# Kernel tuning notes

Measured on AMD Instinct MI355X. Metric: run time of the kernel, lower is better.

## Reference

```python
import jax, jax.numpy as jnp
import numpy as np
import math

D_INPUT = 1024
D_Q = 1024
D_K = 1024
D_V = 1024
D_MODEL = 1024
B, S = 4, 2048


def setup_inputs() -> dict:
    key = jax.random.key(0)
    ks = jax.random.split(key, 9)
    sc = 0.02
    return {
        "x": jax.random.normal(ks[0], (B, S, D_INPUT), dtype=jnp.float32),
        "wq": jax.random.normal(ks[1], (D_INPUT, D_Q), dtype=jnp.float32) * sc,
        "bq": jnp.zeros((D_Q,), dtype=jnp.float32),
        "wk": jax.random.normal(ks[2], (D_INPUT, D_K), dtype=jnp.float32) * sc,
        "bk": jnp.zeros((D_K,), dtype=jnp.float32),
        "wv": jax.random.normal(ks[3], (D_INPUT, D_V), dtype=jnp.float32) * sc,
        "bv": jnp.zeros((D_V,), dtype=jnp.float32),
        "wp": jax.random.normal(ks[4], (D_V, D_MODEL), dtype=jnp.float32) * sc,
        "bp": jnp.zeros((D_MODEL,), dtype=jnp.float32),
    }


def reference(x, wq, bq, wk, bk, wv, bv, wp, bp):
    scale = math.sqrt(D_K)  # NOTE: original MULTIPLIES by sqrt(d_k)
    q = x @ wq + bq  # [B,S,Dq]
    k = x @ wk + bk  # [B,S,Dk]
    v = x @ wv + bv  # [B,S,Dv]
    scores = jnp.einsum('bsd,btd->bst', q, k) * scale
    p_attn = jax.nn.softmax(scores, axis=-1)
    # dropout: inference mode (training=False) -> identity
    context = jnp.einsum('bst,btd->bsd', p_attn, v)
    output = context @ wp + bp
    return (output, p_attn)
```

## Files before the change

kernel.cpp:

```cpp
#include <hip/hip_runtime.h>

typedef unsigned short u16;
typedef short bf16x8 __attribute__((ext_vector_type(8)));
typedef float floatx4 __attribute__((ext_vector_type(4)));

static __device__ __forceinline__ u16 f2bf(float f) {
  unsigned int u = __float_as_uint(f);
  unsigned int lsb = (u >> 16) & 1u;
  u += 0x7FFFu + lsb;
  return (u16)(u >> 16);
}
static __device__ __forceinline__ float bf2f(u16 u) {
  return __uint_as_float(((unsigned int)u) << 16);
}

static __device__ __forceinline__ void gl_lds16(const u16* g, u16* l) {
  __builtin_amdgcn_global_load_lds(
      (const __attribute__((address_space(1))) void*)g,
      (__attribute__((address_space(3))) void*)l, 16, 0, 0);
}

__global__ __launch_bounds__(256)
void prep_all(const float* __restrict__ wq, const float* __restrict__ wk,
              const float* __restrict__ wv, const float* __restrict__ wp,
              const float* __restrict__ bq, const float* __restrict__ bk,
              const float* __restrict__ x,
              u16* __restrict__ qkThi, u16* __restrict__ qkTlo,
              u16* __restrict__ wvThi, u16* __restrict__ wpThi,
              float* __restrict__ bqk,
              u16* __restrict__ xhi, u16* __restrict__ xlo,
              u16* __restrict__ xThi) {
  __shared__ float t[32][33];
  const int z = blockIdx.z;
  const int tid = threadIdx.x;
  const int lr = tid >> 3;
  const int lc = (tid & 7) * 4;

  if (z == 4) {
    if (blockIdx.y == 0 && blockIdx.x < 8) {
      const int i = blockIdx.x * 256 + tid;
      bqk[i] = (i < 1024) ? bq[i] : bk[i - 1024];
    }
    return;
  }

  if (z >= 5) {
    const int r0 = ((z - 5) * 32 + blockIdx.y) * 32;
    const int c0 = blockIdx.x * 32;
    float4 v = *(const float4*)(x + (size_t)(r0 + lr) * 1024 + c0 + lc);
    float f[4] = {v.x, v.y, v.z, v.w};
    t[lr][lc + 0] = v.x; t[lr][lc + 1] = v.y; t[lr][lc + 2] = v.z; t[lr][lc + 3] = v.w;
    u16 ph[4], pl[4];
#pragma unroll
    for (int j = 0; j < 4; j++) {
      ph[j] = f2bf(f[j]);
      pl[j] = f2bf(f[j] - bf2f(ph[j]));
    }
    const size_t o = (size_t)(r0 + lr) * 1024 + c0 + lc;
    *(uint2*)(xhi + o) = *(uint2*)ph;
    *(uint2*)(xlo + o) = *(uint2*)pl;
    __syncthreads();
    u16 pt[4];
#pragma unroll
    for (int j = 0; j < 4; j++) pt[j] = f2bf(t[lc + j][lr]);
    const int b = r0 >> 11, rt = r0 & 2047;
    *(uint2*)(xThi + (size_t)b * (1024 * 2048) + (size_t)(c0 + lr) * 2048 + rt + lc) =
        *(uint2*)pt;
    return;
  }

  const float* in = (z == 0) ? wq : (z == 1) ? wk : (z == 2) ? wv : wp;
  u16* hi = (z == 2) ? wvThi : (z == 3) ? wpThi : (qkThi + (size_t)z * 1024 * 1024);
  u16* lo = (z == 0) ? qkTlo : (z == 1) ? (qkTlo + 1024 * 1024) : (u16*)nullptr;
  const int want_lo = (z < 2);

  const int r0 = blockIdx.y * 32, c0 = blockIdx.x * 32;
  float4 v = *(const float4*)(in + (size_t)(r0 + lr) * 1024 + c0 + lc);
  t[lr][lc + 0] = v.x; t[lr][lc + 1] = v.y; t[lr][lc + 2] = v.z; t[lr][lc + 3] = v.w;
  __syncthreads();
  u16 ph[4], pl[4];
#pragma unroll
  for (int j = 0; j < 4; j++) {
    float f = t[lc + j][lr];
    ph[j] = f2bf(f);
    if (want_lo) pl[j] = f2bf(f - bf2f(ph[j]));
  }
  const size_t o = (size_t)(c0 + lr) * 1024 + r0 + lc;
  *(uint2*)(hi + o) = *(uint2*)ph;
  if (want_lo) *(uint2*)(lo + o) = *(uint2*)pl;
}

template<int KB, int ASP, int BSP, int OM, int HB>
__global__ __launch_bounds__(256)
void gemm_mfma(const u16* __restrict__ Ahi, const u16* __restrict__ Alo,
               const u16* __restrict__ Bhi, const u16* __restrict__ Blo,
               const float* __restrict__ bias,
               void* __restrict__ C0, void* __restrict__ C1,
               void* __restrict__ C2, void* __restrict__ C3,
               int N, int K, int lda, int ldb, int ldc,
               long long aB, long long bB, long long cB, float scale) {
  constexpr int CM = KB / 8 - 1;
  constexpr int RPI = 512 / KB;
  constexpr int NI = KB / 16;
  constexpr int PL = 128 * KB;
  __shared__ __align__(16) u16 As[(1 + ASP) * PL];
  __shared__ __align__(16) u16 Bs[(1 + BSP) * PL];

  const int bz = blockIdx.z;
  const u16* A0 = Ahi + (size_t)bz * aB;
  const u16* A1 = ASP ? (Alo + (size_t)bz * aB) : (const u16*)nullptr;
  const u16* B0 = Bhi + (size_t)bz * bB;
  const u16* B1 = BSP ? (Blo + (size_t)bz * bB) : (const u16*)nullptr;

  const int m0 = blockIdx.y * 128;
  const int n0 = blockIdx.x * 128;
  const int tid = threadIdx.x;
  const int w = tid >> 6;
  const int L = tid & 63;
  const int rr = L & 15, quad = L >> 4;
  const int wm = (w >> 1) * 64, wn = (w & 1) * 64;

  const int lrow = (KB == 32) ? (L >> 2) : (L >> 3);
  const int c3 = (L & CM) ^ ((L >> 3) & CM);
  const int srow = w * 32 + lrow;
  u16* stA = &As[w * 32 * KB];
  u16* stB = &Bs[w * 32 * KB];
  const u16* gA0 = A0 + (size_t)(m0 + srow) * lda + c3 * 8;
  const u16* gA1 = ASP ? A1 + (size_t)(m0 + srow) * lda + c3 * 8 : (const u16*)nullptr;
  const u16* gB0 = B0 + (size_t)(n0 + srow) * ldb + c3 * 8;
  const u16* gB1 = BSP ? B1 + (size_t)(n0 + srow) * ldb + c3 * 8 : (const u16*)nullptr;

  floatx4 acc[4][4] = {};

  for (int k0 = 0; k0 < K; k0 += KB) {
#pragma unroll
    for (int q = 0; q < NI; q++) {
      gl_lds16(gA0 + k0 + (size_t)q * RPI * lda, stA + q * 512);
      gl_lds16(gB0 + k0 + (size_t)q * RPI * ldb, stB + q * 512);
    }
    if (ASP) {
#pragma unroll
      for (int q = 0; q < NI; q++)
        gl_lds16(gA1 + k0 + (size_t)q * RPI * lda, stA + PL + q * 512);
    }
    if (BSP) {
#pragma unroll
      for (int q = 0; q < NI; q++)
        gl_lds16(gB1 + k0 + (size_t)q * RPI * ldb, stB + PL + q * 512);
    }
    __syncthreads();

#pragma unroll
    for (int s = 0; s < KB / 32; s++) {
      const int pcb = ((KB == 32) ? (quad ^ ((rr >> 1) & 3))
                                  : ((s * 4 + quad) ^ (rr & 7))) * 8;
      bf16x8 a0[4], a1[4], b0[4], b1[4];
#pragma unroll
      for (int i = 0; i < 4; i++) {
        const int arow = wm + i * 16 + rr;
        const int brow = wn + i * 16 + rr;
        a0[i] = *(const bf16x8*)&As[arow * KB + pcb];
        b0[i] = *(const bf16x8*)&Bs[brow * KB + pcb];
        if (ASP) a1[i] = *(const bf16x8*)&As[PL + arow * KB + pcb];
        if (BSP) b1[i] = *(const bf16x8*)&Bs[PL + brow * KB + pcb];
      }
#pragma unroll
      for (int i = 0; i < 4; i++) {
#pragma unroll
        for (int j = 0; j < 4; j++) {
          acc[i][j] = __builtin_amdgcn_mfma_f32_16x16x32_bf16(a0[i], b0[j], acc[i][j], 0, 0, 0);
          if (ASP && BSP) {
            acc[i][j] = __builtin_amdgcn_mfma_f32_16x16x32_bf16(a0[i], b1[j], acc[i][j], 0, 0, 0);
            acc[i][j] = __builtin_amdgcn_mfma_f32_16x16x32_bf16(a1[i], b0[j], acc[i][j], 0, 0, 0);
          }
        }
      }
    }
    __syncthreads();
  }

#pragma unroll
  for (int i = 0; i < 4; i++) {
    const int mbase = m0 + wm + i * 16 + quad * 4;
#pragma unroll
    for (int j = 0; j < 4; j++) {
      const int col = n0 + wn + j * 16 + rr;
      float bvs = 0.f;
      if (HB) bvs = bias[col];
      if (OM == 5) {
        u16* hi; u16* lo;
        if (col < 1024) { hi = (u16*)C0; lo = (u16*)C1; }
        else            { hi = (u16*)C2; lo = (u16*)C3; }
        const int cc = col & 1023;
#pragma unroll
        for (int ii = 0; ii < 4; ii++) {
          const float v = acc[i][j][ii] + bvs;
          const size_t idx = (size_t)(mbase + ii) * 1024 + cc;
          const u16 h = f2bf(v);
          hi[idx] = h;
          lo[idx] = f2bf(v - bf2f(h));
        }
      } else {
        u16* Cb = (u16*)C0 + (size_t)bz * cB;
        float* Cf = (float*)C0 + (size_t)bz * cB;
        u16* Cl = (OM == 1) ? ((u16*)C1 + (size_t)bz * cB) : (u16*)nullptr;
#pragma unroll
        for (int ii = 0; ii < 4; ii++) {
          const float v = acc[i][j][ii] * scale + bvs;
          const size_t idx = (size_t)(mbase + ii) * ldc + col;
          if (OM == 0) {
            Cb[idx] = f2bf(v);
          } else if (OM == 1) {
            const u16 h = f2bf(v);
            Cb[idx] = h;
            Cl[idx] = f2bf(v - bf2f(h));
          } else {
            Cf[idx] = v;
          }
        }
      }
    }
  }
}

template<int OM>
__global__ __launch_bounds__(512, 2)
void gemm8(const u16* __restrict__ Ahi, const u16* __restrict__ Alo,
           const u16* __restrict__ Bhi, const u16* __restrict__ Blo,
           const float* __restrict__ bias,
           void* __restrict__ C0, void* __restrict__ C1,
           void* __restrict__ C2, void* __restrict__ C3,
           long long aB, long long bB, long long cB, float scale) {
  __shared__ __align__(16) u16 As[4 * 8192];
  __shared__ __align__(16) u16 Bs[4 * 8192];

  const int gx = gridDim.x, gy = gridDim.y, gz = gridDim.z;
  const int flat = blockIdx.x + gx * (blockIdx.y + gy * blockIdx.z);
  const int nwg = gx * gy * gz;
  const int lg = (flat & 7) * (nwg >> 3) + (flat >> 3);
  const int bx = lg % gx;
  const int by = (lg / gx) % gy;
  const int bz = lg / (gx * gy);

  const int m0 = by * 256, n0 = bx * 256;
  const u16* pAhi = Ahi + (size_t)bz * aB;
  const u16* pAlo = Alo + (size_t)bz * aB;
  const u16* pBhi = Bhi + (size_t)bz * bB;
  const u16* pBlo = Blo + (size_t)bz * bB;

  const int tid = threadIdx.x;
  const int w = tid >> 6;
  const int L = tid & 63;
  const int rr = L & 15, quad = L >> 4;
  const int wm = (w >> 2) * 128;
  const int wn = (w & 3) * 64;

  const int rbase = w * 16 + (L >> 2);
  const int coff = (((L & 3) ^ ((L >> 3) & 3)) << 3);
  const int arow = (m0 + rbase) * 1024 + coff;
  const int brow = (n0 + rbase) * 1024 + coff;
  u16* const ldA = As + w * 512;
  u16* const ldB = Bs + w * 512;

  const int aoff = ((wm + rr) << 5) + ((quad ^ ((rr >> 1) & 3)) << 3);
  const int boff = ((wn + rr) << 5) + ((quad ^ ((rr >> 1) & 3)) << 3);

  auto stageA = [&](int H) {
    const int kt = H >> 1;
    const u16* src = (kt < 32) ? pAhi : pAlo;
    const int koff = ((kt & 15) << 6) + ((H & 1) << 5);
    const u16* g = src + arow + koff;
    u16* l = ldA + (H & 3) * 8192;
    gl_lds16(g, l);
    gl_lds16(g + 128 * 1024, l + 4096);
  };
  auto stageB = [&](int H) {
    const int kt = H >> 1;
    const u16* src = (kt < 16) ? pBhi : (kt < 32) ? pBlo : pBhi;
    const int koff = ((kt & 15) << 6) + ((H & 1) << 5);
    const u16* g = src + brow + koff;
    u16* l = ldB + (H & 3) * 8192;
    gl_lds16(g, l);
    gl_lds16(g + 128 * 1024, l + 4096);
  };

  floatx4 acc[8][4] = {};

#define PAIR(H, SB2, SA3, VM)                                                  \
  {                                                                            \
    __builtin_amdgcn_sched_barrier(0);                                         \
    const u16* ab = As + ((H) & 3) * 8192 + aoff;                              \
    const u16* bb = Bs + ((H) & 3) * 8192 + boff;                              \
    bf16x8 a[8], b0, b1, b2, b3;                                               \
    _Pragma("unroll")                                                          \
    for (int i = 0; i < 8; i++) a[i] = *(const bf16x8*)(ab + i * 512);         \
    b0 = *(const bf16x8*)(bb);                                                 \
    b1 = *(const bf16x8*)(bb + 512);                                           \
    b2 = *(const bf16x8*)(bb + 1024);                                          \
    b3 = *(const bf16x8*)(bb + 1536);                                          \
    if (SB2) stageB((H) + 2);                                                  \
    __builtin_amdgcn_s_barrier();                                              \
    asm volatile("s_waitcnt lgkmcnt(2)");                                      \
    __builtin_amdgcn_s_setprio(1);                                             \
    _Pragma("unroll")                                                          \
    for (int i = 0; i < 8; i++) {                                              \
      acc[i][0] = __builtin_amdgcn_mfma_f32_16x16x32_bf16(a[i], b0, acc[i][0], 0, 0, 0); \
      acc[i][1] = __builtin_amdgcn_mfma_f32_16x16x32_bf16(a[i], b1, acc[i][1], 0, 0, 0); \
    }                                                                          \
    __builtin_amdgcn_s_setprio(0);                                             \
    __builtin_amdgcn_s_barrier();                                              \
    if (SA3) stageA((H) + 3);                                                  \
    asm volatile("s_waitcnt lgkmcnt(0)");                                      \
    __builtin_amdgcn_s_setprio(1);                                             \
    _Pragma("unroll")                                                          \
    for (int i = 0; i < 8; i++) {                                              \
      acc[i][2] = __builtin_amdgcn_mfma_f32_16x16x32_bf16(a[i], b2, acc[i][2], 0, 0, 0); \
      acc[i][3] = __builtin_amdgcn_mfma_f32_16x16x32_bf16(a[i], b3, acc[i][3], 0, 0, 0); \
    }                                                                          \
    __builtin_amdgcn_s_setprio(0);                                             \
    if ((VM) == 6) asm volatile("s_waitcnt vmcnt(6)");                         \
    else if ((VM) == 4) asm volatile("s_waitcnt vmcnt(4)");                    \
    else if ((VM) == 0) asm volatile("s_waitcnt vmcnt(0)");                    \
    __builtin_amdgcn_s_barrier();                                              \
  }

  stageA(0); stageB(0); stageA(1); stageB(1); stageA(2);
  asm volatile("s_waitcnt vmcnt(6)");
  __builtin_amdgcn_s_barrier();

  for (int H = 0; H <= 92; ++H)
    PAIR(H, true, true, 6);
  PAIR(93, true, false, 4);
  PAIR(94, false, false, 0);
  PAIR(95, false, false, -1);
#undef PAIR

#pragma unroll
  for (int i = 0; i < 8; i++) {
    const int mb = m0 + wm + i * 16 + quad * 4;
#pragma unroll
    for (int j = 0; j < 4; j++) {
      const int col = n0 + wn + j * 16 + rr;
      if (OM == 5) {
        u16* hi; u16* lo;
        if (col < 1024) { hi = (u16*)C0; lo = (u16*)C1; }
        else            { hi = (u16*)C2; lo = (u16*)C3; }
        const int cc = col & 1023;
        const float bvs = bias[col];
#pragma unroll
        for (int ii = 0; ii < 4; ii++) {
          const float v = acc[i][j][ii] + bvs;
          const size_t idx = (size_t)(mb + ii) * 1024 + cc;
          const u16 h = f2bf(v);
          hi[idx] = h;
          lo[idx] = f2bf(v - bf2f(h));
        }
      } else {
        float* Cf = (float*)C0 + (size_t)bz * cB;
#pragma unroll
        for (int ii = 0; ii < 4; ii++)
          Cf[(size_t)(mb + ii) * 2048 + col] = acc[i][j][ii] * scale;
      }
    }
  }
}

__global__ __launch_bounds__(256)
void softmax_rows(float* __restrict__ S, u16* __restrict__ Pb) {
  const int row = blockIdx.x;
  float* s = S + (size_t)row * 2048;
  const int tid = threadIdx.x;
  const int w = tid >> 6;
  __shared__ float redm[4];
  __shared__ float reds[4];

  float v[8];
  float mx = -1e30f;
#pragma unroll
  for (int i = 0; i < 8; i++) {
    v[i] = s[tid + 256 * i];
    mx = fmaxf(mx, v[i]);
  }
#pragma unroll
  for (int o = 32; o > 0; o >>= 1) mx = fmaxf(mx, __shfl_xor(mx, o, 64));
  if ((tid & 63) == 0) redm[w] = mx;
  __syncthreads();
  mx = fmaxf(fmaxf(redm[0], redm[1]), fmaxf(redm[2], redm[3]));

  float sum = 0.f;
#pragma unroll
  for (int i = 0; i < 8; i++) {
    v[i] = __expf(v[i] - mx);
    sum += v[i];
  }
#pragma unroll
  for (int o = 32; o > 0; o >>= 1) sum += __shfl_xor(sum, o, 64);
  if ((tid & 63) == 0) reds[w] = sum;
  __syncthreads();
  sum = reds[0] + reds[1] + reds[2] + reds[3];
  const float rs = 1.0f / sum;
#pragma unroll
  for (int i = 0; i < 8; i++) {
    const float p = v[i] * rs;
    s[tid + 256 * i] = p;
    Pb[(size_t)row * 2048 + tid + 256 * i] = f2bf(p);
  }
}

extern "C" void kernel_launch(void* const* d_in, const int* in_sizes, int n_in,
                              void* d_out, int out_size, void* d_ws, size_t ws_size,
                              hipStream_t stream) {
  const float* x  = (const float*)d_in[0];
  const float* wq = (const float*)d_in[1];
  const float* bq = (const float*)d_in[2];
  const float* wk = (const float*)d_in[3];
  const float* bk = (const float*)d_in[4];
  const float* wv = (const float*)d_in[5];
  const float* bv = (const float*)d_in[6];
  const float* wp = (const float*)d_in[7];
  const float* bp = (const float*)d_in[8];

  const size_t MB = 1024 * 1024;
  char* ws = (char*)d_ws;
  u16* qkThi = (u16*)(ws + 0 * MB);
  u16* qkTlo = (u16*)(ws + 4 * MB);
  u16* wvThi = (u16*)(ws + 8 * MB);
  u16* wpThi = (u16*)(ws + 10 * MB);
  float* bqk = (float*)(ws + 12 * MB);
  u16* xhi   = (u16*)(ws + 13 * MB);
  u16* xlo   = (u16*)(ws + 29 * MB);
  u16* qhi   = (u16*)(ws + 45 * MB);
  u16* qlo   = (u16*)(ws + 61 * MB);
  u16* khi   = (u16*)(ws + 77 * MB);
  u16* klo   = (u16*)(ws + 93 * MB);
  u16* xThi  = (u16*)(ws + 109 * MB);
  u16* pbf   = khi;
  u16* px    = qhi;
  u16* ctx   = qlo;

  float* outp = (float*)d_out;
  float* scf  = (float*)d_out + 8388608;

  const dim3 blk(256);

  prep_all<<<dim3(32, 32, 13), blk, 0, stream>>>(
      wq, wk, wv, wp, bq, bk, x, qkThi, qkTlo, wvThi, wpThi, bqk, xhi, xlo, xThi);

  gemm8<5><<<dim3(8, 32, 1), dim3(512), 0, stream>>>(
      xhi, xlo, qkThi, qkTlo, bqk, qhi, qlo, khi, klo, 0, 0, 0, 1.0f);

  gemm8<2><<<dim3(8, 8, 4), dim3(512), 0, stream>>>(
      qhi, qlo, khi, klo, nullptr, scf, nullptr, nullptr, nullptr,
      2048LL * 1024, 2048LL * 1024, 2048LL * 2048, 32.0f);

  softmax_rows<<<dim3(8192), blk, 0, stream>>>(scf, pbf);

  gemm_mfma<64, 0, 0, 0, 0><<<dim3(8, 16, 4), blk, 0, stream>>>(
      pbf, nullptr, xThi, nullptr, nullptr, px, nullptr, nullptr, nullptr,
      1024, 2048, 2048, 2048, 1024,
      2048LL * 2048, 1024LL * 2048, 2048LL * 1024, 1.0f);

  gemm_mfma<64, 0, 0, 0, 1><<<dim3(8, 64, 1), blk, 0, stream>>>(
      px, nullptr, wvThi, nullptr, bv, ctx, nullptr, nullptr, nullptr,
      1024, 1024, 1024, 1024, 1024, 0, 0, 0, 1.0f);

  gemm_mfma<64, 0, 0, 2, 1><<<dim3(8, 64, 1), blk, 0, stream>>>(
      ctx, nullptr, wpThi, nullptr, bp, outp, nullptr, nullptr, nullptr,
      1024, 1024, 1024, 1024, 1024, 0, 0, 0, 1.0f);
}
```

Measured before the change: 453.8 us.

## Double-buffer LDS-to-register fragments and prefetch next K-slice during MFMAs

Restructures the GEMM main loop so the A fragments and first B pair for the next K-slice are read from LDS into alternating register sets while the current MFMAs run. One mid-step s_barrier is removed, the explicit lgkmcnt waits are dropped, and the vmcnt thresholds are retuned to match. The aim is to hide LDS read latency and cut barrier stalls, at the cost of more VGPRs and possible occupancy loss. Correctness now depends on the compiler inserting the LDS waits that were previously explicit.

```diff
diff --git a/kernel.cpp b/kernel.cpp
--- a/kernel.cpp
+++ b/kernel.cpp
@@ -285,55 +285,66 @@
   };
 
   floatx4 acc[8][4] = {};
-
-#define PAIR(H, SB2, SA3, VM)                                                  \
+  bf16x8 aE[8], aO[8], b01E[2], b01O[2], b23[2];
+
+#define RD_SET(slot, A_, B_)                                                   \
+  {                                                                            \
+    const u16* ab_ = As + ((slot) & 3) * 8192 + aoff;                          \
+    const u16* bb_ = Bs + ((slot) & 3) * 8192 + boff;                          \
+    _Pragma("unroll")                                                          \
+    for (int i = 0; i < 8; i++) A_[i] = *(const bf16x8*)(ab_ + i * 512);       \
+    B_[0] = *(const bf16x8*)(bb_);                                             \
+    B_[1] = *(const bf16x8*)(bb_ + 512);                                       \
+  }
+
+#define PAIRX(H, AC, B01C, AN, B01N, SB2, SA3, RDN, VM)                        \
   {                                                                            \
     __builtin_amdgcn_sched_barrier(0);                                         \
-    const u16* ab = As + ((H) & 3) * 8192 + aoff;                              \
-    const u16* bb = Bs + ((H) & 3) * 8192 + boff;                              \
-    bf16x8 a[8], b0, b1, b2, b3;                                               \
-    _Pragma("unroll")                                                          \
-    for (int i = 0; i < 8; i++) a[i] = *(const bf16x8*)(ab + i * 512);         \
-    b0 = *(const bf16x8*)(bb);                                                 \
-    b1 = *(const bf16x8*)(bb + 512);                                           \
-    b2 = *(const bf16x8*)(bb + 1024);                                          \
-    b3 = *(const bf16x8*)(bb + 1536);                                          \
+    {                                                                          \
+      const u16* bb_ = Bs + ((H) & 3) * 8192 + boff;                           \
+      b23[0] = *(const bf16x8*)(bb_ + 1024);                                   \
+      b23[1] = *(const bf16x8*)(bb_ + 1536);                                   \
+    }                                                                          \
     if (SB2) stageB((H) + 2);                                                  \
-    __builtin_amdgcn_s_barrier();                                              \
-    asm volatile("s_waitcnt lgkmcnt(2)");                                      \
+    __builtin_amdgcn_sched_barrier(0);                                         \
     __builtin_amdgcn_s_setprio(1);                                             \
     _Pragma("unroll")                                                          \
     for (int i = 0; i < 8; i++) {                                              \
-      acc[i][0] = __builtin_amdgcn_mfma_f32_16x16x32_bf16(a[i], b0, acc[i][0], 0, 0, 0); \
-      acc[i][1] = __builtin_amdgcn_mfma_f32_16x16x32_bf16(a[i], b1, acc[i][1], 0, 0, 0); \
+      acc[i][0] = __builtin_amdgcn_mfma_f32_16x16x32_bf16(AC[i], B01C[0], acc[i][0], 0, 0, 0); \
+      acc[i][1] = __builtin_amdgcn_mfma_f32_16x16x32_bf16(AC[i], B01C[1], acc[i][1], 0, 0, 0); \
     }                                                                          \
     __builtin_amdgcn_s_setprio(0);                                             \
-    __builtin_amdgcn_s_barrier();                                              \
+    __builtin_amdgcn_sched_barrier(0);                                         \
+    if (RDN) RD_SET((H) + 1, AN, B01N);                                        \
     if (SA3) stageA((H) + 3);                                                  \
-    asm volatile("s_waitcnt lgkmcnt(0)");                                      \
+    __builtin_amdgcn_sched_barrier(0);                                         \
     __builtin_amdgcn_s_setprio(1);                                             \
     _Pragma("unroll")                                                          \
     for (int i = 0; i < 8; i++) {                                              \
-      acc[i][2] = __builtin_amdgcn_mfma_f32_16x16x32_bf16(a[i], b2, acc[i][2], 0, 0, 0); \
-      acc[i][3] = __builtin_amdgcn_mfma_f32_16x16x32_bf16(a[i], b3, acc[i][3], 0, 0, 0); \
+      acc[i][2] = __builtin_amdgcn_mfma_f32_16x16x32_bf16(AC[i], b23[0], acc[i][2], 0, 0, 0); \
+      acc[i][3] = __builtin_amdgcn_mfma_f32_16x16x32_bf16(AC[i], b23[1], acc[i][3], 0, 0, 0); \
     }                                                                          \
     __builtin_amdgcn_s_setprio(0);                                             \
-    if ((VM) == 6) asm volatile("s_waitcnt vmcnt(6)");                         \
-    else if ((VM) == 4) asm volatile("s_waitcnt vmcnt(4)");                    \
+    if ((VM) == 2) asm volatile("s_waitcnt vmcnt(2)");                         \
     else if ((VM) == 0) asm volatile("s_waitcnt vmcnt(0)");                    \
     __builtin_amdgcn_s_barrier();                                              \
   }
 
   stageA(0); stageB(0); stageA(1); stageB(1); stageA(2);
-  asm volatile("s_waitcnt vmcnt(6)");
+  asm volatile("s_waitcnt vmcnt(2)");
   __builtin_amdgcn_s_barrier();
-
-  for (int H = 0; H <= 92; ++H)
-    PAIR(H, true, true, 6);
-  PAIR(93, true, false, 4);
-  PAIR(94, false, false, 0);
-  PAIR(95, false, false, -1);
-#undef PAIR
+  RD_SET(0, aE, b01E);
+
+  for (int H = 0; H < 92; H += 2) {
+    PAIRX(H,     aE, b01E, aO, b01O, true, true, true, 2);
+    PAIRX(H + 1, aO, b01O, aE, b01E, true, true, true, 2);
+  }
+  PAIRX(92, aE, b01E, aO, b01O, true,  true,  true,  2);
+  PAIRX(93, aO, b01O, aE, b01E, true,  false, true,  0);
+  PAIRX(94, aE, b01E, aO, b01O, false, false, true,  -1);
+  PAIRX(95, aO, b01O, aE, b01E, false, false, false, -1);
+#undef PAIRX
+#undef RD_SET
 
 #pragma unroll
   for (int i = 0; i < 8; i++) {
```

New measurement: 436.8 us. -3.7%, faster.
